# Optimization experiments

Measured on AMD Instinct MI355X. Metric: run time of the kernel, lower is better.

Reference implementation:

```python
import jax, jax.numpy as jnp
import numpy as np

B, T, D, E, H, K = 4, 1024, 1024, 8, 4096, 2
N = B * T
EPS_LN = 1e-5
EPS_W = 1e-8
BAL_W = 0.01


def setup_inputs() -> dict:
    key = jax.random.key(0)
    ks = jax.random.split(key, 5)
    sc = 0.02
    return {
        "x": jax.random.normal(ks[0], (B, T, D), jnp.float32),
        "ln_gamma": jnp.ones((D,), jnp.float32),
        "ln_beta": jnp.zeros((D,), jnp.float32),
        "gate_w": jax.random.normal(ks[1], (D, E), jnp.float32) * sc,
        "w1": jax.random.normal(ks[2], (E, D, H), jnp.float32) * sc,
        "b1": jnp.zeros((E, H), jnp.float32),
        "w2": jax.random.normal(ks[3], (E, H, D), jnp.float32) * sc,
        "b2": jnp.zeros((E, D), jnp.float32),
    }


def reference(x, ln_gamma, ln_beta, gate_w, w1, b1, w2, b2):
    # LayerNorm (pre-norm), residual kept on raw x
    mu = jnp.mean(x, axis=-1, keepdims=True)
    var = jnp.var(x, axis=-1, keepdims=True)
    xn = (x - mu) * jax.lax.rsqrt(var + EPS_LN) * ln_gamma + ln_beta

    xf = xn.reshape(N, D)

    # Router (oscillator_state=None path): token gate only, k = top_k
    logits = xf @ gate_w                         # (N, E)
    router_probs = jax.nn.softmax(logits, axis=-1)
    top_w, top_i = jax.lax.top_k(router_probs, K)  # (N, K)
    top_w = top_w / (jnp.sum(top_w, axis=-1, keepdims=True) + EPS_W)

    # Dense per-token gate matrix: gates[n, e] = sum of top-k weights routed to e
    gates = jnp.zeros((N, E), xf.dtype).at[jnp.arange(N)[:, None], top_i].add(top_w)

    # Per-expert FFN (computed densely for all tokens, combined by sparse gates)
    h = jax.nn.gelu(jnp.einsum("nd,edh->enh", xf, w1) + b1[:, None, :], approximate=False)
    expert_out = jnp.einsum("enh,ehd->end", h, w2) + b2[:, None, :]  # (E, N, D)
    moe = jnp.einsum("ne,end->nd", gates, expert_out)

    output = x + moe.reshape(B, T, D)

    # Load-balance auxiliary loss
    counts = jnp.zeros((E,), xf.dtype).at[top_i.reshape(-1)].add(1.0)
    fraction = counts / N
    balance_loss = BAL_W * E * jnp.sum(fraction * jnp.mean(router_probs, axis=0))

    return output, balance_loss, router_probs
```

## Files before the change

### kernel.cpp

```cpp
#include <hip/hip_runtime.h>
#include <hip/hip_bf16.h>
#include <math.h>

#define DI   1024
#define EI   8
#define HI   4096
#define NI   4096

typedef __bf16 bf16x8 __attribute__((ext_vector_type(8)));
typedef float  f32x4  __attribute__((ext_vector_type(4)));

__device__ __forceinline__ unsigned short f2bf(float f) {
  union { float f; unsigned u; } c; c.f = f;
  unsigned r = c.u + 0x7FFF + ((c.u >> 16) & 1);
  return (unsigned short)(r >> 16);
}

__device__ __forceinline__ void async16(const void* g, void* l) {
  __builtin_amdgcn_global_load_lds(
      (const __attribute__((address_space(1))) void*)g,
      (__attribute__((address_space(3))) void*)l, 16, 0, 0);
}

__global__ __launch_bounds__(256) void ln_router_k(
    const float* __restrict__ x, const float* __restrict__ gamma,
    const float* __restrict__ beta, const float* __restrict__ gw,
    unsigned short* __restrict__ xnbf, float* __restrict__ probs_out,
    int* __restrict__ pairs, float2* __restrict__ gates2)
{
  const int t = threadIdx.x, lane = t & 63, wid = t >> 6;
  const int n = blockIdx.x * 4 + wid;

  const float4* xr = (const float4*)(x + (size_t)n * DI);
  float4 v[4];
  #pragma unroll
  for (int j = 0; j < 4; j++) v[j] = xr[lane * 4 + j];

  float s = 0.f, q = 0.f;
  #pragma unroll
  for (int j = 0; j < 4; j++) {
    s += v[j].x + v[j].y + v[j].z + v[j].w;
    q += v[j].x * v[j].x + v[j].y * v[j].y + v[j].z * v[j].z + v[j].w * v[j].w;
  }
  #pragma unroll
  for (int off = 1; off < 64; off <<= 1) {
    s += __shfl_xor(s, off);
    q += __shfl_xor(q, off);
  }
  const float mu = s * (1.0f / DI);
  const float rs = rsqrtf(q * (1.0f / DI) - mu * mu + 1e-5f);

  const float4* gr = (const float4*)gamma;
  const float4* br = (const float4*)beta;
  float xl[16];
  #pragma unroll
  for (int j = 0; j < 4; j++) {
    const float4 g4 = gr[lane * 4 + j];
    const float4 b4 = br[lane * 4 + j];
    xl[4 * j + 0] = (v[j].x - mu) * rs * g4.x + b4.x;
    xl[4 * j + 1] = (v[j].y - mu) * rs * g4.y + b4.y;
    xl[4 * j + 2] = (v[j].z - mu) * rs * g4.z + b4.z;
    xl[4 * j + 3] = (v[j].w - mu) * rs * g4.w + b4.w;
  }
  unsigned u[8];
  #pragma unroll
  for (int j = 0; j < 8; j++)
    u[j] = (unsigned)f2bf(xl[2 * j]) | ((unsigned)f2bf(xl[2 * j + 1]) << 16);
  uint4* dst = (uint4*)(xnbf + (size_t)n * DI + lane * 16);
  uint4 d0; d0.x = u[0]; d0.y = u[1]; d0.z = u[2]; d0.w = u[3];
  uint4 d1; d1.x = u[4]; d1.y = u[5]; d1.z = u[6]; d1.w = u[7];
  dst[0] = d0; dst[1] = d1;

  float p[8];
  #pragma unroll
  for (int e = 0; e < 8; e++) p[e] = 0.f;
  #pragma unroll
  for (int j = 0; j < 16; j++) {
    const float4* grow = (const float4*)(gw + (size_t)(lane * 16 + j) * EI);
    const float4 ga = grow[0], gb = grow[1];
    const float xv = xl[j];
    p[0] += xv * ga.x; p[1] += xv * ga.y; p[2] += xv * ga.z; p[3] += xv * ga.w;
    p[4] += xv * gb.x; p[5] += xv * gb.y; p[6] += xv * gb.z; p[7] += xv * gb.w;
  }
  #pragma unroll
  for (int e = 0; e < 8; e++)
    #pragma unroll
    for (int off = 1; off < 64; off <<= 1) p[e] += __shfl_xor(p[e], off);

  if (lane == 0) {
    float pm = -1e30f;
    #pragma unroll
    for (int e = 0; e < 8; e++) pm = fmaxf(pm, p[e]);
    float pr[8], ps = 0.f;
    #pragma unroll
    for (int e = 0; e < 8; e++) { pr[e] = expf(p[e] - pm); ps += pr[e]; }
    const float inv = 1.0f / ps;
    #pragma unroll
    for (int e = 0; e < 8; e++) {
      pr[e] *= inv;
      probs_out[(size_t)n * EI + e] = pr[e];
    }
    int i0 = 0; float m0 = pr[0];
    #pragma unroll
    for (int e = 1; e < 8; e++) if (pr[e] > m0) { m0 = pr[e]; i0 = e; }
    int i1 = -1; float m1 = -1e30f;
    #pragma unroll
    for (int e = 0; e < 8; e++) if (e != i0 && pr[e] > m1) { m1 = pr[e]; i1 = e; }
    const float ssum = m0 + m1 + 1e-8f;
    pairs[n] = i0 | (i1 << 8);
    float2 g2; g2.x = m0 / ssum; g2.y = m1 / ssum;
    gates2[n] = g2;
  }
}

__global__ __launch_bounds__(1024) void build_lists_k(
    const int* __restrict__ pairs, const float2* __restrict__ gates2,
    const float* __restrict__ probs, int* __restrict__ counts,
    int* __restrict__ offs, int* __restrict__ tok_list,
    float* __restrict__ gate_list, float* __restrict__ out_bal)
{
  __shared__ int cnt[8];
  __shared__ int cur[8];
  __shared__ float wps[16][8];
  __shared__ float ps[8];
  const int t = threadIdx.x, lane = t & 63, wid = t >> 6;
  if (t < 8) cnt[t] = 0;
  __syncthreads();

  float acc[8];
  #pragma unroll
  for (int e = 0; e < 8; e++) acc[e] = 0.f;
  for (int n = t; n < NI; n += 1024) {
    const int pr = pairs[n];
    atomicAdd(&cnt[pr & 255], 1);
    atomicAdd(&cnt[pr >> 8], 1);
    const float4* prow = (const float4*)(probs + (size_t)n * EI);
    const float4 a = prow[0], b = prow[1];
    acc[0] += a.x; acc[1] += a.y; acc[2] += a.z; acc[3] += a.w;
    acc[4] += b.x; acc[5] += b.y; acc[6] += b.z; acc[7] += b.w;
  }
  #pragma unroll
  for (int e = 0; e < 8; e++)
    #pragma unroll
    for (int off = 1; off < 64; off <<= 1) acc[e] += __shfl_xor(acc[e], off);
  if (lane == 0)
    #pragma unroll
    for (int e = 0; e < 8; e++) wps[wid][e] = acc[e];
  __syncthreads();
  if (t < 8) {
    float sm = 0.f;
    for (int w = 0; w < 16; w++) sm += wps[w][t];
    ps[t] = sm;
  }
  __syncthreads();
  if (t == 0) {
    int off = 0; float bl = 0.f;
    for (int e = 0; e < 8; e++) {
      offs[e] = off; cur[e] = off; counts[e] = cnt[e];
      bl += (float)cnt[e] * ps[e];
      off += cnt[e];
    }
    *out_bal = 0.01f * 8.0f * bl / ((float)NI * (float)NI);
  }
  __syncthreads();
  for (int n = t; n < NI; n += 1024) {
    const int pr = pairs[n];
    const float2 g = gates2[n];
    const int p0 = atomicAdd(&cur[pr & 255], 1);
    tok_list[p0] = n; gate_list[p0] = g.x;
    const int p1 = atomicAdd(&cur[pr >> 8], 1);
    tok_list[p1] = n; gate_list[p1] = g.y;
  }
}

__global__ __launch_bounds__(256) void transpose_cvt_k(
    const float* __restrict__ in, unsigned short* __restrict__ out, int R, int C)
{
  __shared__ float tile[64][65];
  const size_t eoff = (size_t)blockIdx.z * (size_t)R * (size_t)C;
  const int c0 = blockIdx.x * 64, r0 = blockIdx.y * 64;
  const int tx = threadIdx.x & 63, ty = threadIdx.x >> 6;
  #pragma unroll
  for (int ii = 0; ii < 16; ii++) {
    int i = ty + ii * 4;
    tile[i][tx] = in[eoff + (size_t)(r0 + i) * C + (c0 + tx)];
  }
  __syncthreads();
  #pragma unroll
  for (int ii = 0; ii < 16; ii++) {
    int i = ty + ii * 4;
    out[eoff + (size_t)(c0 + i) * R + (r0 + tx)] = f2bf(tile[tx][i]);
  }
}

__global__ __launch_bounds__(256) void copy_x_k(const float* __restrict__ x, float* __restrict__ out)
{
  const size_t i = (size_t)blockIdx.x * 256 + threadIdx.x;
  ((float4*)out)[i] = ((const float4*)x)[i];
}

__global__ __launch_bounds__(256) void ffn1_k(
    const unsigned short* __restrict__ xnbf, const unsigned short* __restrict__ w1t,
    const float* __restrict__ b1, unsigned short* __restrict__ hbuf,
    const int* __restrict__ tok_list, const int* __restrict__ counts,
    const int* __restrict__ offsets)
{
  const int e = blockIdx.z;
  const int cnt = counts[e];
  const int mt = blockIdx.y;
  if (mt * 128 >= cnt) return;
  const int n0 = blockIdx.x * 128;
  const int t = threadIdx.x, lane = t & 63, w = t >> 6;
  const int wm = w & 1, wn = w >> 1;
  __shared__ __align__(16) unsigned short As[128 * 64];
  __shared__ __align__(16) unsigned short Bs[128 * 64];

  const int sub = lane >> 3, kc = (lane & 7) * 8;
  const int eoff = offsets[e];
  const unsigned short* baseA[4];
  const unsigned short* baseB[4];
  #pragma unroll
  for (int r = 0; r < 4; r++) {
    int row = (w << 5) + r * 8 + sub;
    int idx = mt * 128 + row; if (idx > cnt - 1) idx = cnt - 1;
    int tok = tok_list[eoff + idx];
    baseA[r] = xnbf + (size_t)tok * DI + kc;
    baseB[r] = w1t + (size_t)e * HI * DI + (size_t)(n0 + row) * DI + kc;
  }

  f32x4 acc[4][4];
  const f32x4 zz = {0.f, 0.f, 0.f, 0.f};
  #pragma unroll
  for (int i = 0; i < 4; i++)
    #pragma unroll
    for (int j = 0; j < 4; j++) acc[i][j] = zz;

  const int mrow = (wm << 6) + (lane & 15);
  const int nrow = (wn << 6) + (lane & 15);
  const int kq = (lane >> 4) * 8;

  for (int k0 = 0; k0 < DI; k0 += 64) {
    __syncthreads();
    #pragma unroll
    for (int r = 0; r < 4; r++) {
      async16(baseA[r] + k0, &As[((w << 5) + r * 8) * 64]);
      async16(baseB[r] + k0, &Bs[((w << 5) + r * 8) * 64]);
    }
    __syncthreads();
    #pragma unroll
    for (int kk = 0; kk < 2; kk++) {
      bf16x8 af[4], bfr[4];
      #pragma unroll
      for (int mi = 0; mi < 4; mi++)
        af[mi] = *(const bf16x8*)&As[(mrow + mi * 16) * 64 + kk * 32 + kq];
      #pragma unroll
      for (int ni = 0; ni < 4; ni++)
        bfr[ni] = *(const bf16x8*)&Bs[(nrow + ni * 16) * 64 + kk * 32 + kq];
      #pragma unroll
      for (int mi = 0; mi < 4; mi++)
        #pragma unroll
        for (int ni = 0; ni < 4; ni++)
          acc[mi][ni] = __builtin_amdgcn_mfma_f32_16x16x32_bf16(af[mi], bfr[ni], acc[mi][ni], 0, 0, 0);
    }
  }

  const int hb = eoff + mt * 128;
  #pragma unroll
  for (int ni = 0; ni < 4; ni++) {
    const int col = n0 + (wn << 6) + ni * 16 + (lane & 15);
    const float bias = b1[e * HI + col];
    #pragma unroll
    for (int mi = 0; mi < 4; mi++) {
      #pragma unroll
      for (int rg = 0; rg < 4; rg++) {
        const int rowl = (wm << 6) + mi * 16 + ((lane >> 4) << 2) + rg;
        if (mt * 128 + rowl < cnt) {
          float vv = acc[mi][ni][rg] + bias;
          vv = 0.5f * vv * (1.0f + erff(vv * 0.70710678118f));
          hbuf[(size_t)(hb + rowl) * HI + col] = f2bf(vv);
        }
      }
    }
  }
}

__global__ __launch_bounds__(256) void ffn2_k(
    const unsigned short* __restrict__ hbuf, const unsigned short* __restrict__ w2t,
    const float* __restrict__ b2, float* __restrict__ out,
    const int* __restrict__ tok_list, const float* __restrict__ gate_list,
    const int* __restrict__ counts, const int* __restrict__ offsets)
{
  const int e = blockIdx.z;
  const int cnt = counts[e];
  const int mt = blockIdx.y;
  if (mt * 128 >= cnt) return;
  const int n0 = blockIdx.x * 128;
  const int t = threadIdx.x, lane = t & 63, w = t >> 6;
  const int wm = w & 1, wn = w >> 1;
  __shared__ __align__(16) unsigned short As[128 * 64];
  __shared__ __align__(16) unsigned short Bs[128 * 64];

  const int sub = lane >> 3, kc = (lane & 7) * 8;
  const int eoff = offsets[e];
  const int hb = eoff + mt * 128;
  const unsigned short* baseA[4];
  const unsigned short* baseB[4];
  #pragma unroll
  for (int r = 0; r < 4; r++) {
    int row = (w << 5) + r * 8 + sub;
    baseA[r] = hbuf + (size_t)(hb + row) * HI + kc;
    baseB[r] = w2t + (size_t)e * DI * HI + (size_t)(n0 + row) * HI + kc;
  }

  f32x4 acc[4][4];
  const f32x4 zz = {0.f, 0.f, 0.f, 0.f};
  #pragma unroll
  for (int i = 0; i < 4; i++)
    #pragma unroll
    for (int j = 0; j < 4; j++) acc[i][j] = zz;

  const int mrow = (wm << 6) + (lane & 15);
  const int nrow = (wn << 6) + (lane & 15);
  const int kq = (lane >> 4) * 8;

  for (int k0 = 0; k0 < HI; k0 += 64) {
    __syncthreads();
    #pragma unroll
    for (int r = 0; r < 4; r++) {
      async16(baseA[r] + k0, &As[((w << 5) + r * 8) * 64]);
      async16(baseB[r] + k0, &Bs[((w << 5) + r * 8) * 64]);
    }
    __syncthreads();
    #pragma unroll
    for (int kk = 0; kk < 2; kk++) {
      bf16x8 af[4], bfr[4];
      #pragma unroll
      for (int mi = 0; mi < 4; mi++)
        af[mi] = *(const bf16x8*)&As[(mrow + mi * 16) * 64 + kk * 32 + kq];
      #pragma unroll
      for (int ni = 0; ni < 4; ni++)
        bfr[ni] = *(const bf16x8*)&Bs[(nrow + ni * 16) * 64 + kk * 32 + kq];
      #pragma unroll
      for (int mi = 0; mi < 4; mi++)
        #pragma unroll
        for (int ni = 0; ni < 4; ni++)
          acc[mi][ni] = __builtin_amdgcn_mfma_f32_16x16x32_bf16(af[mi], bfr[ni], acc[mi][ni], 0, 0, 0);
    }
  }

  float bias[4];
  #pragma unroll
  for (int ni = 0; ni < 4; ni++)
    bias[ni] = b2[e * DI + n0 + (wn << 6) + ni * 16 + (lane & 15)];
  #pragma unroll
  for (int mi = 0; mi < 4; mi++) {
    #pragma unroll
    for (int rg = 0; rg < 4; rg++) {
      const int rowl = (wm << 6) + mi * 16 + ((lane >> 4) << 2) + rg;
      const int gidx = mt * 128 + rowl;
      if (gidx < cnt) {
        const int tok = tok_list[eoff + gidx];
        const float gte = gate_list[eoff + gidx];
        float* orow = out + (size_t)tok * DI;
        #pragma unroll
        for (int ni = 0; ni < 4; ni++) {
          const int col = n0 + (wn << 6) + ni * 16 + (lane & 15);
          atomicAdd(orow + col, (acc[mi][ni][rg] + bias[ni]) * gte);
        }
      }
    }
  }
}

extern "C" void kernel_launch(void* const* d_in, const int* in_sizes, int n_in,
                              void* d_out, int out_size, void* d_ws, size_t ws_size,
                              hipStream_t stream)
{
  const float* x   = (const float*)d_in[0];
  const float* gam = (const float*)d_in[1];
  const float* bet = (const float*)d_in[2];
  const float* gw  = (const float*)d_in[3];
  const float* w1  = (const float*)d_in[4];
  const float* b1  = (const float*)d_in[5];
  const float* w2  = (const float*)d_in[6];
  const float* b2  = (const float*)d_in[7];
  float* out = (float*)d_out;

  char* ws = (char*)d_ws;
  int*    counts = (int*)(ws + 0);
  int*    offs   = (int*)(ws + 64);
  int*    pairs  = (int*)(ws + 1024);
  float2* gates2 = (float2*)(ws + 20480);
  int*    tok    = (int*)(ws + 57344);
  float*  gate   = (float*)(ws + 90112);
  unsigned short* xnbf = (unsigned short*)(ws + 262656);
  unsigned short* wt   = (unsigned short*)(ws + 8651264);
  unsigned short* hbuf = (unsigned short*)(ws + 75760128);

  float* bal_out   = out + (size_t)NI * DI;
  float* probs_out = bal_out + 1;

  ln_router_k<<<NI / 4, 256, 0, stream>>>(x, gam, bet, gw, xnbf, probs_out, pairs, gates2);
  build_lists_k<<<1, 1024, 0, stream>>>(pairs, gates2, probs_out, counts, offs, tok, gate, bal_out);
  transpose_cvt_k<<<dim3(HI / 64, DI / 64, EI), 256, 0, stream>>>(w1, wt, DI, HI);
  copy_x_k<<<(NI * DI / 4) / 256, 256, 0, stream>>>(x, out);
  ffn1_k<<<dim3(HI / 128, NI / 128, EI), 256, 0, stream>>>(xnbf, wt, b1, hbuf, tok, counts, offs);
  transpose_cvt_k<<<dim3(DI / 64, HI / 64, EI), 256, 0, stream>>>(w2, wt, HI, DI);
  ffn2_k<<<dim3(DI / 128, NI / 128, EI), 256, 0, stream>>>(hbuf, wt, b2, out, tok, gate, counts, offs);
}
```

Measured before the change: 729.0 us.

## Swizzle LDS tiles, vectorize weight transpose, replace atomic scatter with combine kernel

Applies an XOR swizzle to the LDS k-chunk layout in both expert GEMMs to reduce bank conflicts on fragment reads. Rewrites the weight transpose/convert kernel to use float4 loads and 16-byte packed bf16 stores. When the workspace is large enough, ffn2 writes per-slot expert outputs to a buffer and a new combine kernel gathers the two slots per token with the residual, replacing the x copy and the float atomics. The combine path costs an extra fp32 buffer write and read, and depends on the workspace size check.

```diff
diff --git a/kernel.cpp b/kernel.cpp
--- a/kernel.cpp
+++ b/kernel.cpp
@@ -117,7 +117,8 @@
     const int* __restrict__ pairs, const float2* __restrict__ gates2,
     const float* __restrict__ probs, int* __restrict__ counts,
     int* __restrict__ offs, int* __restrict__ tok_list,
-    float* __restrict__ gate_list, float* __restrict__ out_bal)
+    float* __restrict__ gate_list, int2* __restrict__ ipos,
+    float* __restrict__ out_bal)
 {
   __shared__ int cnt[8];
   __shared__ int cur[8];
@@ -170,6 +171,8 @@
     tok_list[p0] = n; gate_list[p0] = g.x;
     const int p1 = atomicAdd(&cur[pr >> 8], 1);
     tok_list[p1] = n; gate_list[p1] = g.y;
+    int2 ip; ip.x = p0; ip.y = p1;
+    ipos[n] = ip;
   }
 }
 
@@ -179,17 +182,33 @@
   __shared__ float tile[64][65];
   const size_t eoff = (size_t)blockIdx.z * (size_t)R * (size_t)C;
   const int c0 = blockIdx.x * 64, r0 = blockIdx.y * 64;
-  const int tx = threadIdx.x & 63, ty = threadIdx.x >> 6;
-  #pragma unroll
-  for (int ii = 0; ii < 16; ii++) {
-    int i = ty + ii * 4;
-    tile[i][tx] = in[eoff + (size_t)(r0 + i) * C + (c0 + tx)];
+  const int t = threadIdx.x;
+  {
+    const int col = (t & 15) * 4;
+    #pragma unroll
+    for (int ii = 0; ii < 4; ii++) {
+      const int row = (t >> 4) + ii * 16;
+      const float4 v = *(const float4*)(in + eoff + (size_t)(r0 + row) * C + c0 + col);
+      tile[row][col + 0] = v.x; tile[row][col + 1] = v.y;
+      tile[row][col + 2] = v.z; tile[row][col + 3] = v.w;
+    }
   }
   __syncthreads();
-  #pragma unroll
-  for (int ii = 0; ii < 16; ii++) {
-    int i = ty + ii * 4;
-    out[eoff + (size_t)(c0 + i) * R + (r0 + tx)] = f2bf(tile[tx][i]);
+  {
+    const int grp = t & 7;
+    #pragma unroll
+    for (int jj = 0; jj < 2; jj++) {
+      const int orow = (t >> 3) + jj * 32;
+      unsigned short vs[8];
+      #pragma unroll
+      for (int u = 0; u < 8; u++) vs[u] = f2bf(tile[grp * 8 + u][orow]);
+      uint4 pk;
+      pk.x = (unsigned)vs[0] | ((unsigned)vs[1] << 16);
+      pk.y = (unsigned)vs[2] | ((unsigned)vs[3] << 16);
+      pk.z = (unsigned)vs[4] | ((unsigned)vs[5] << 16);
+      pk.w = (unsigned)vs[6] | ((unsigned)vs[7] << 16);
+      *(uint4*)(out + eoff + (size_t)(c0 + orow) * R + r0 + grp * 8) = pk;
+    }
   }
 }
 
@@ -215,7 +234,8 @@
   __shared__ __align__(16) unsigned short As[128 * 64];
   __shared__ __align__(16) unsigned short Bs[128 * 64];
 
-  const int sub = lane >> 3, kc = (lane & 7) * 8;
+  const int sub = lane >> 3;
+  const int kc = (((lane & 7) ^ sub) * 8);
   const int eoff = offsets[e];
   const unsigned short* baseA[4];
   const unsigned short* baseB[4];
@@ -237,7 +257,8 @@
 
   const int mrow = (wm << 6) + (lane & 15);
   const int nrow = (wn << 6) + (lane & 15);
-  const int kq = (lane >> 4) * 8;
+  const int ksw[2] = { (((lane >> 4) ^ (lane & 7)) * 8),
+                       ((((lane >> 4) + 4) ^ (lane & 7)) * 8) };
 
   for (int k0 = 0; k0 < DI; k0 += 64) {
     __syncthreads();
@@ -249,13 +270,14 @@
     __syncthreads();
     #pragma unroll
     for (int kk = 0; kk < 2; kk++) {
+      const int ko = ksw[kk];
       bf16x8 af[4], bfr[4];
       #pragma unroll
       for (int mi = 0; mi < 4; mi++)
-        af[mi] = *(const bf16x8*)&As[(mrow + mi * 16) * 64 + kk * 32 + kq];
+        af[mi] = *(const bf16x8*)&As[(mrow + mi * 16) * 64 + ko];
       #pragma unroll
       for (int ni = 0; ni < 4; ni++)
-        bfr[ni] = *(const bf16x8*)&Bs[(nrow + ni * 16) * 64 + kk * 32 + kq];
+        bfr[ni] = *(const bf16x8*)&Bs[(nrow + ni * 16) * 64 + ko];
       #pragma unroll
       for (int mi = 0; mi < 4; mi++)
         #pragma unroll
@@ -288,7 +310,8 @@
     const unsigned short* __restrict__ hbuf, const unsigned short* __restrict__ w2t,
     const float* __restrict__ b2, float* __restrict__ out,
     const int* __restrict__ tok_list, const float* __restrict__ gate_list,
-    const int* __restrict__ counts, const int* __restrict__ offsets)
+    const int* __restrict__ counts, const int* __restrict__ offsets,
+    float* __restrict__ eo)
 {
   const int e = blockIdx.z;
   const int cnt = counts[e];
@@ -300,7 +323,8 @@
   __shared__ __align__(16) unsigned short As[128 * 64];
   __shared__ __align__(16) unsigned short Bs[128 * 64];
 
-  const int sub = lane >> 3, kc = (lane & 7) * 8;
+  const int sub = lane >> 3;
+  const int kc = (((lane & 7) ^ sub) * 8);
   const int eoff = offsets[e];
   const int hb = eoff + mt * 128;
   const unsigned short* baseA[4];
@@ -321,7 +345,8 @@
 
   const int mrow = (wm << 6) + (lane & 15);
   const int nrow = (wn << 6) + (lane & 15);
-  const int kq = (lane >> 4) * 8;
+  const int ksw[2] = { (((lane >> 4) ^ (lane & 7)) * 8),
+                       ((((lane >> 4) + 4) ^ (lane & 7)) * 8) };
 
   for (int k0 = 0; k0 < HI; k0 += 64) {
     __syncthreads();
@@ -333,13 +358,14 @@
     __syncthreads();
     #pragma unroll
     for (int kk = 0; kk < 2; kk++) {
+      const int ko = ksw[kk];
       bf16x8 af[4], bfr[4];
       #pragma unroll
       for (int mi = 0; mi < 4; mi++)
-        af[mi] = *(const bf16x8*)&As[(mrow + mi * 16) * 64 + kk * 32 + kq];
+        af[mi] = *(const bf16x8*)&As[(mrow + mi * 16) * 64 + ko];
       #pragma unroll
       for (int ni = 0; ni < 4; ni++)
-        bfr[ni] = *(const bf16x8*)&Bs[(nrow + ni * 16) * 64 + kk * 32 + kq];
+        bfr[ni] = *(const bf16x8*)&Bs[(nrow + ni * 16) * 64 + ko];
       #pragma unroll
       for (int mi = 0; mi < 4; mi++)
         #pragma unroll
@@ -352,24 +378,63 @@
   #pragma unroll
   for (int ni = 0; ni < 4; ni++)
     bias[ni] = b2[e * DI + n0 + (wn << 6) + ni * 16 + (lane & 15)];
-  #pragma unroll
-  for (int mi = 0; mi < 4; mi++) {
-    #pragma unroll
-    for (int rg = 0; rg < 4; rg++) {
-      const int rowl = (wm << 6) + mi * 16 + ((lane >> 4) << 2) + rg;
-      const int gidx = mt * 128 + rowl;
-      if (gidx < cnt) {
-        const int tok = tok_list[eoff + gidx];
-        const float gte = gate_list[eoff + gidx];
-        float* orow = out + (size_t)tok * DI;
-        #pragma unroll
-        for (int ni = 0; ni < 4; ni++) {
-          const int col = n0 + (wn << 6) + ni * 16 + (lane & 15);
-          atomicAdd(orow + col, (acc[mi][ni][rg] + bias[ni]) * gte);
+
+  if (eo) {
+    #pragma unroll
+    for (int mi = 0; mi < 4; mi++) {
+      #pragma unroll
+      for (int rg = 0; rg < 4; rg++) {
+        const int rowl = (wm << 6) + mi * 16 + ((lane >> 4) << 2) + rg;
+        const int gidx = mt * 128 + rowl;
+        if (gidx < cnt) {
+          float* erow = eo + (size_t)(hb + rowl) * DI;
+          #pragma unroll
+          for (int ni = 0; ni < 4; ni++) {
+            const int col = n0 + (wn << 6) + ni * 16 + (lane & 15);
+            erow[col] = acc[mi][ni][rg] + bias[ni];
+          }
         }
       }
     }
-  }
+  } else {
+    #pragma unroll
+    for (int mi = 0; mi < 4; mi++) {
+      #pragma unroll
+      for (int rg = 0; rg < 4; rg++) {
+        const int rowl = (wm << 6) + mi * 16 + ((lane >> 4) << 2) + rg;
+        const int gidx = mt * 128 + rowl;
+        if (gidx < cnt) {
+          const int tok = tok_list[eoff + gidx];
+          const float gte = gate_list[eoff + gidx];
+          float* orow = out + (size_t)tok * DI;
+          #pragma unroll
+          for (int ni = 0; ni < 4; ni++) {
+            const int col = n0 + (wn << 6) + ni * 16 + (lane & 15);
+            atomicAdd(orow + col, (acc[mi][ni][rg] + bias[ni]) * gte);
+          }
+        }
+      }
+    }
+  }
+}
+
+__global__ __launch_bounds__(256) void combine_k(
+    const float* __restrict__ x, const float* __restrict__ eo,
+    const int2* __restrict__ ipos, const float2* __restrict__ gates2,
+    float* __restrict__ out)
+{
+  const int n = blockIdx.x, t = threadIdx.x;
+  const int2 pp = ipos[n];
+  const float2 gg = gates2[n];
+  const float4 a = ((const float4*)(x  + (size_t)n    * DI))[t];
+  const float4 b = ((const float4*)(eo + (size_t)pp.x * DI))[t];
+  const float4 c = ((const float4*)(eo + (size_t)pp.y * DI))[t];
+  float4 r;
+  r.x = a.x + gg.x * b.x + gg.y * c.x;
+  r.y = a.y + gg.x * b.y + gg.y * c.y;
+  r.z = a.z + gg.x * b.z + gg.y * c.z;
+  r.w = a.w + gg.x * b.w + gg.y * c.w;
+  ((float4*)(out + (size_t)n * DI))[t] = r;
 }
 
 extern "C" void kernel_launch(void* const* d_in, const int* in_sizes, int n_in,
@@ -393,18 +458,24 @@
   float2* gates2 = (float2*)(ws + 20480);
   int*    tok    = (int*)(ws + 57344);
   float*  gate   = (float*)(ws + 90112);
+  int2*   ipos   = (int2*)(ws + 122880);
   unsigned short* xnbf = (unsigned short*)(ws + 262656);
   unsigned short* wt   = (unsigned short*)(ws + 8651264);
   unsigned short* hbuf = (unsigned short*)(ws + 75760128);
+  const bool use_eo = (ws_size >= 177472000ull);
+  float* eo = use_eo ? (float*)(ws + 143917568) : (float*)nullptr;
 
   float* bal_out   = out + (size_t)NI * DI;
   float* probs_out = bal_out + 1;
 
   ln_router_k<<<NI / 4, 256, 0, stream>>>(x, gam, bet, gw, xnbf, probs_out, pairs, gates2);
-  build_lists_k<<<1, 1024, 0, stream>>>(pairs, gates2, probs_out, counts, offs, tok, gate, bal_out);
+  build_lists_k<<<1, 1024, 0, stream>>>(pairs, gates2, probs_out, counts, offs, tok, gate, ipos, bal_out);
   transpose_cvt_k<<<dim3(HI / 64, DI / 64, EI), 256, 0, stream>>>(w1, wt, DI, HI);
-  copy_x_k<<<(NI * DI / 4) / 256, 256, 0, stream>>>(x, out);
+  if (!use_eo)
+    copy_x_k<<<(NI * DI / 4) / 256, 256, 0, stream>>>(x, out);
   ffn1_k<<<dim3(HI / 128, NI / 128, EI), 256, 0, stream>>>(xnbf, wt, b1, hbuf, tok, counts, offs);
   transpose_cvt_k<<<dim3(DI / 64, HI / 64, EI), 256, 0, stream>>>(w2, wt, HI, DI);
-  ffn2_k<<<dim3(DI / 128, NI / 128, EI), 256, 0, stream>>>(hbuf, wt, b2, out, tok, gate, counts, offs);
-}
+  ffn2_k<<<dim3(DI / 128, NI / 128, EI), 256, 0, stream>>>(hbuf, wt, b2, out, tok, gate, counts, offs, eo);
+  if (use_eo)
+    combine_k<<<NI, 256, 0, stream>>>(x, eo, ipos, gates2, out);
+}
```

After: 659.9 us. -9.5%, faster.
